# Performance work log

Measured on AMD Instinct MI355X. Metric: run time of the kernel, lower is better.

## Reference

```python
import jax, jax.numpy as jnp
import numpy as np

N_NODES = 50000
N_EDGES = 800000
IN_DIM = 128
HID_DIM = 256
OUT_DIM = 128


def _sage_conv(x, edge_index, W_l, b_l, W_r):
    """PyG SAGEConv with mean aggregation:
       out_i = W_l @ mean_{j in N(i)} x_j + b_l + W_r @ x_i
    edge_index: [2, E] with row 0 = source j, row 1 = target i."""
    src, dst = edge_index[0], edge_index[1]
    n = x.shape[0]
    # gather source features along edges, scatter-sum into targets
    msg_sum = jax.ops.segment_sum(x[src], dst, num_segments=n)  # [N, D]
    deg = jax.ops.segment_sum(jnp.ones((src.shape[0],), dtype=x.dtype), dst,
                              num_segments=n)                    # [N]
    msg_mean = msg_sum / jnp.maximum(deg, 1.0)[:, None]
    return msg_mean @ W_l.T + b_l + x @ W_r.T


def setup_inputs() -> dict:
    key = jax.random.key(0)
    ks = jax.random.split(key, 8)
    x = jax.random.normal(ks[0], (N_NODES, IN_DIM), dtype=jnp.float32)
    edge_index = jax.random.randint(ks[1], (2, N_EDGES), 0, N_NODES, dtype=jnp.int64)
    # glorot-ish scaled params
    def w(k, shape):
        fan_in = shape[-1]
        return jax.random.normal(k, shape, dtype=jnp.float32) / np.sqrt(fan_in)
    W1_l = w(ks[2], (HID_DIM, IN_DIM))
    W1_r = w(ks[3], (HID_DIM, IN_DIM))
    b1 = jnp.zeros((HID_DIM,), dtype=jnp.float32)
    W2_l = w(ks[4], (OUT_DIM, HID_DIM))
    W2_r = w(ks[5], (OUT_DIM, HID_DIM))
    b2 = jnp.zeros((OUT_DIM,), dtype=jnp.float32)
    return {"x": x, "edge_index": edge_index,
            "W1_l": W1_l, "b1": b1, "W1_r": W1_r,
            "W2_l": W2_l, "b2": b2, "W2_r": W2_r}


def reference(x, edge_index, W1_l, b1, W1_r, W2_l, b2, W2_r):
    h = _sage_conv(x, edge_index, W1_l, b1, W1_r)
    h = jax.nn.relu(h)
    # dropout(p=0.3) is identity in inference mode
    out = _sage_conv(h, edge_index, W2_l, b2, W2_r)
    return out
```

## Files before the change

kernel.cpp:

```cpp
#include <hip/hip_runtime.h>
#include <stdint.h>

#define NN 50000
#define NE 800000
#define NBK 512
#define NPB 98
#define BUCKCAP 2048

typedef __bf16 bf16x8 __attribute__((ext_vector_type(8)));
typedef float  f32x4  __attribute__((ext_vector_type(4)));

__device__ __forceinline__ unsigned short f2bf(float f) {
    unsigned int u = __float_as_uint(f);
    unsigned int r = (u + 0x7fffu + ((u >> 16) & 1u)) >> 16;
    return (unsigned short)r;
}
__device__ __forceinline__ float bf_lo(unsigned int v) { return __uint_as_float(v << 16); }
__device__ __forceinline__ float bf_hi(unsigned int v) { return __uint_as_float(v & 0xffff0000u); }

__device__ __forceinline__ void gl_lds16(const void* g, void* l) {
    __builtin_amdgcn_global_load_lds(
        (const __attribute__((address_space(1))) void*)g,
        (__attribute__((address_space(3))) void*)l, 16, 0, 0);
}

#define FILL_NB 391
#define PACK_NB 512
#define CAST_NB 6250
__global__ __launch_bounds__(256) void mega_kernel(
    const int* __restrict__ edges,
    int* __restrict__ bcur, unsigned int* __restrict__ packed,
    const float* __restrict__ x,
    const float* __restrict__ W1l, const float* __restrict__ W1r,
    const float* __restrict__ W2l, const float* __restrict__ W2r,
    unsigned short* __restrict__ x_bf,
    unsigned short* __restrict__ B1, unsigned short* __restrict__ B2) {
    __shared__ int hist[NBK];
    __shared__ int scn[NBK];
    __shared__ int gbase[NBK];
    __shared__ int lcur[NBK];
    __shared__ int ps[256];
    __shared__ unsigned int sortbuf[2048];
    __shared__ int gaddrbuf[2048];
    __shared__ int nz;
    int b = blockIdx.x;
    int t = threadIdx.x;
    if (b < FILL_NB) {
        const int E = NE;
        if (t == 0) nz = 0;
        hist[t] = 0; hist[t + 256] = 0;
        __syncthreads();
        int accv = 0;
        for (int i = t; i < 512; i += 256) accv |= edges[2 * i + 1];
        if (accv) atomicOr(&nz, 1);
        __syncthreads();
        int f = nz ? 0 : 1;

        int blockbase = b * 2048;
        int nedge = E - blockbase; if (nedge > 2048) nedge = 2048;
        unsigned int pk[8]; int bk[8];
#pragma unroll
        for (int u = 0; u < 8; ++u) {
            int lin = u * 256 + t;
            bk[u] = -1;
            if (lin < nedge) {
                int e = blockbase + lin;
                int src = edges[(size_t)e << f];
                int dst = edges[(size_t)(E + e) << f];
                int bb = dst / NPB;
                pk[u] = (unsigned int)src | ((unsigned int)(dst - bb * NPB) << 16);
                bk[u] = bb;
                atomicAdd(&hist[bb], 1);
            }
        }
        __syncthreads();
        int h0 = hist[2 * t], h1 = hist[2 * t + 1];
        int s = h0 + h1;
        ps[t] = s;
        __syncthreads();
        for (int off = 1; off < 256; off <<= 1) {
            int v = (t >= off) ? ps[t - off] : 0;
            __syncthreads();
            ps[t] += v;
            __syncthreads();
        }
        int excl = ps[t] - s;
        scn[2 * t] = excl;
        scn[2 * t + 1] = excl + h0;
        if (h0) gbase[2 * t] = atomicAdd(&bcur[2 * t], h0);
        if (h1) gbase[2 * t + 1] = atomicAdd(&bcur[2 * t + 1], h1);
        lcur[2 * t] = excl;
        lcur[2 * t + 1] = excl + h0;
        __syncthreads();
#pragma unroll
        for (int u = 0; u < 8; ++u) {
            if (bk[u] >= 0) {
                int p = atomicAdd(&lcur[bk[u]], 1);
                sortbuf[p] = pk[u];
                int off = gbase[bk[u]] + (p - scn[bk[u]]);
                gaddrbuf[p] = (off < BUCKCAP) ? (bk[u] * BUCKCAP + off) : -1;
            }
        }
        __syncthreads();
        for (int j = t; j < nedge; j += 256) {
            int a = gaddrbuf[j];
            if (a >= 0) packed[a] = sortbuf[j];
        }
    } else if (b < FILL_NB + PACK_NB) {
        int idx = (b - FILL_NB) * 256 + t;
        if (idx < 65536) {
            int o = idx >> 8, k = idx & 255;
            float v = (k < 128) ? W1l[o * 128 + k] : W1r[o * 128 + (k - 128)];
            B1[idx] = f2bf(v);
        } else {
            int j = idx - 65536;
            int o = j >> 8, k = j & 255;
            float v = (o < 128) ? W2l[o * 256 + k] : W2r[(o - 128) * 256 + k];
            B2[j] = f2bf(v);
        }
    } else {
        int i4 = (b - FILL_NB - PACK_NB) * 256 + t;
        float4 v = *(const float4*)(x + (size_t)i4 * 4);
        uint2 p;
        p.x = (unsigned int)f2bf(v.x) | ((unsigned int)f2bf(v.y) << 16);
        p.y = (unsigned int)f2bf(v.z) | ((unsigned int)f2bf(v.w) << 16);
        *(uint2*)(x_bf + (size_t)i4 * 4) = p;
    }
}

__global__ __launch_bounds__(256) void pass2_kernel(
    const unsigned int* __restrict__ packed, const int* __restrict__ bcur,
    int* __restrict__ nbr, int* __restrict__ row_start, int* __restrict__ deg) {
    __shared__ int hist[NPB];
    __shared__ int scn[NPB];
    __shared__ int lcur[NPB];
    int b = blockIdx.x;
    int t = threadIdx.x;
    int ne = bcur[b]; if (ne > BUCKCAP) ne = BUCKCAP;
    if (t < NPB) hist[t] = 0;
    __syncthreads();
    const unsigned int* pb = packed + (size_t)b * BUCKCAP;
    for (int j = t; j < ne; j += 256) atomicAdd(&hist[pb[j] >> 16], 1);
    __syncthreads();
    if (t == 0) {
        int a = 0;
        for (int i = 0; i < NPB; ++i) { scn[i] = a; a += hist[i]; }
    }
    __syncthreads();
    if (t < NPB) lcur[t] = scn[t];
    __syncthreads();
    for (int j = t; j < ne; j += 256) {
        unsigned int w = pb[j];
        int p = atomicAdd(&lcur[w >> 16], 1);
        nbr[(size_t)b * BUCKCAP + p] = (int)(w & 0xffffu);
    }
    if (t < NPB) {
        int node = b * NPB + t;
        if (node < NN) {
            row_start[node] = b * BUCKCAP + scn[t];
            deg[node] = hist[t];
        }
    }
}

__global__ __launch_bounds__(256) void agg1_kernel(
    const unsigned short* __restrict__ X, const int* __restrict__ row_start,
    const int* __restrict__ deg, const int* __restrict__ nbr,
    unsigned short* __restrict__ mean) {
    int node = blockIdx.x * 16 + (threadIdx.x >> 4);
    int l = threadIdx.x & 15;
    if (node >= NN) return;
    int dg = deg[node];
    const int* sl = nbr + row_start[node];
    float a0 = 0.f, a1 = 0.f, a2 = 0.f, a3 = 0.f, a4 = 0.f, a5 = 0.f, a6 = 0.f, a7 = 0.f;
    int i = 0;
    for (; i + 8 <= dg; i += 8) {
        uint4 v[8];
#pragma unroll
        for (int u = 0; u < 8; ++u) {
            int s = sl[i + u];
            v[u] = *(const uint4*)(X + ((size_t)s << 7) + l * 8);
        }
#pragma unroll
        for (int u = 0; u < 8; ++u) {
            a0 += bf_lo(v[u].x); a1 += bf_hi(v[u].x);
            a2 += bf_lo(v[u].y); a3 += bf_hi(v[u].y);
            a4 += bf_lo(v[u].z); a5 += bf_hi(v[u].z);
            a6 += bf_lo(v[u].w); a7 += bf_hi(v[u].w);
        }
    }
    for (; i < dg; ++i) {
        int s = sl[i];
        uint4 v = *(const uint4*)(X + ((size_t)s << 7) + l * 8);
        a0 += bf_lo(v.x); a1 += bf_hi(v.x);
        a2 += bf_lo(v.y); a3 += bf_hi(v.y);
        a4 += bf_lo(v.z); a5 += bf_hi(v.z);
        a6 += bf_lo(v.w); a7 += bf_hi(v.w);
    }
    float inv = 1.0f / (float)(dg > 1 ? dg : 1);
    uint4 p;
    p.x = (unsigned int)f2bf(a0 * inv) | ((unsigned int)f2bf(a1 * inv) << 16);
    p.y = (unsigned int)f2bf(a2 * inv) | ((unsigned int)f2bf(a3 * inv) << 16);
    p.z = (unsigned int)f2bf(a4 * inv) | ((unsigned int)f2bf(a5 * inv) << 16);
    p.w = (unsigned int)f2bf(a6 * inv) | ((unsigned int)f2bf(a7 * inv) << 16);
    *(uint4*)(mean + ((size_t)node << 7) + l * 8) = p;
}

__global__ __launch_bounds__(256) void gemm_mfma(
    const unsigned short* __restrict__ A1, const unsigned short* __restrict__ A2,
    int astr1, int astr2,
    const unsigned short* __restrict__ B,
    const float* __restrict__ biasBF, const float* __restrict__ biasF,
    unsigned short* __restrict__ outBF, float* __restrict__ outF,
    int N, int split, int reluBF) {
    __shared__ unsigned short As[64 * 64];
    __shared__ unsigned short Bs[256 * 64];
    int tid = threadIdx.x;
    int row0 = blockIdx.x * 64;
    int w = tid >> 6, lane = tid & 63;
    int q = lane >> 4, l16 = lane & 15;
    int rc = lane >> 3;
    int gsw = (lane & 7) ^ (rc & 7);

    f32x4 acc[4][4];
#pragma unroll
    for (int r = 0; r < 4; ++r)
#pragma unroll
        for (int c = 0; c < 4; ++c) acc[r][c] = (f32x4){0.f, 0.f, 0.f, 0.f};

    for (int ks = 0; ks < 4; ++ks) {
        int kbase = ks * 64;
        if (ks) __syncthreads();
        const unsigned short* Ap = (ks < 2) ? A1 : A2;
        int astr = (ks < 2) ? astr1 : astr2;
        int koff = (ks & 1) * 64;
#pragma unroll
        for (int cc = 0; cc < 2; ++cc) {
            int c = w * 2 + cc;
            int grow = row0 + c * 8 + rc;
            if (grow > N - 1) grow = N - 1;
            gl_lds16(Ap + (size_t)grow * astr + koff + gsw * 8, &As[c * 512]);
        }
#pragma unroll
        for (int cc = 0; cc < 8; ++cc) {
            int c = w * 8 + cc;
            int n = c * 8 + rc;
            gl_lds16(B + ((size_t)n << 8) + kbase + gsw * 8, &Bs[c * 512]);
        }
        __syncthreads();
#pragma unroll
        for (int k0 = 0; k0 < 64; k0 += 32) {
            int gb = (k0 >> 3) + q;
            int sl = gb ^ (l16 & 7);
            bf16x8 bfrag[4], afrag[4];
#pragma unroll
            for (int c = 0; c < 4; ++c) {
                int row = w * 64 + c * 16 + l16;
                bfrag[c] = *(const bf16x8*)&Bs[row * 64 + sl * 8];
            }
#pragma unroll
            for (int r = 0; r < 4; ++r) {
                int row = r * 16 + l16;
                afrag[r] = *(const bf16x8*)&As[row * 64 + sl * 8];
            }
#pragma unroll
            for (int r = 0; r < 4; ++r)
#pragma unroll
                for (int c = 0; c < 4; ++c)
                    acc[r][c] = __builtin_amdgcn_mfma_f32_16x16x32_bf16(afrag[r], bfrag[c], acc[r][c], 0, 0, 0);
        }
    }

#pragma unroll
    for (int c = 0; c < 4; ++c) {
        int colg = w * 64 + c * 16 + l16;
        bool isBF = (colg < split);
        float bb = 0.f;
        if (isBF) { if (biasBF) bb = biasBF[colg]; }
        else      bb = biasF[colg - split];
#pragma unroll
        for (int r = 0; r < 4; ++r) {
#pragma unroll
            for (int reg = 0; reg < 4; ++reg) {
                int rowg = row0 + r * 16 + q * 4 + reg;
                if (rowg < N) {
                    float v = acc[r][c][reg] + bb;
                    if (isBF) {
                        if (reluBF) v = fmaxf(v, 0.f);
                        outBF[(size_t)rowg * split + colg] = f2bf(v);
                    } else {
                        outF[(size_t)rowg * (256 - split) + (colg - split)] = v;
                    }
                }
            }
        }
    }
}

__global__ __launch_bounds__(256) void agg2_kernel(
    const unsigned short* __restrict__ P, const float* __restrict__ R,
    const int* __restrict__ row_start, const int* __restrict__ deg,
    const int* __restrict__ nbr, float* __restrict__ out) {
    int node = blockIdx.x * 16 + (threadIdx.x >> 4);
    int l = threadIdx.x & 15;
    if (node >= NN) return;
    int dg = deg[node];
    const int* sl = nbr + row_start[node];
    float a0 = 0.f, a1 = 0.f, a2 = 0.f, a3 = 0.f, a4 = 0.f, a5 = 0.f, a6 = 0.f, a7 = 0.f;
    int i = 0;
    for (; i + 8 <= dg; i += 8) {
        uint4 v[8];
#pragma unroll
        for (int u = 0; u < 8; ++u) {
            int s = sl[i + u];
            v[u] = *(const uint4*)(P + ((size_t)s << 7) + l * 8);
        }
#pragma unroll
        for (int u = 0; u < 8; ++u) {
            a0 += bf_lo(v[u].x); a1 += bf_hi(v[u].x);
            a2 += bf_lo(v[u].y); a3 += bf_hi(v[u].y);
            a4 += bf_lo(v[u].z); a5 += bf_hi(v[u].z);
            a6 += bf_lo(v[u].w); a7 += bf_hi(v[u].w);
        }
    }
    for (; i < dg; ++i) {
        int s = sl[i];
        uint4 v = *(const uint4*)(P + ((size_t)s << 7) + l * 8);
        a0 += bf_lo(v.x); a1 += bf_hi(v.x);
        a2 += bf_lo(v.y); a3 += bf_hi(v.y);
        a4 += bf_lo(v.z); a5 += bf_hi(v.z);
        a6 += bf_lo(v.w); a7 += bf_hi(v.w);
    }
    float inv = 1.0f / (float)(dg > 1 ? dg : 1);
    const float* rrow = R + ((size_t)node << 7) + l * 8;
    float4 r0 = *(const float4*)rrow;
    float4 r1 = *(const float4*)(rrow + 4);
    float4 o0, o1;
    o0.x = a0 * inv + r0.x; o0.y = a1 * inv + r0.y;
    o0.z = a2 * inv + r0.z; o0.w = a3 * inv + r0.w;
    o1.x = a4 * inv + r1.x; o1.y = a5 * inv + r1.y;
    o1.z = a6 * inv + r1.z; o1.w = a7 * inv + r1.w;
    float* orow = out + ((size_t)node << 7) + l * 8;
    *(float4*)orow = o0;
    *(float4*)(orow + 4) = o1;
}

extern "C" void kernel_launch(void* const* d_in, const int* in_sizes, int n_in,
                              void* d_out, int out_size, void* d_ws, size_t ws_size,
                              hipStream_t stream) {
    const float* x    = (const float*)d_in[0];
    const int*   edges = (const int*)d_in[1];
    const float* W1_l = (const float*)d_in[2];
    const float* b1   = (const float*)d_in[3];
    const float* W1_r = (const float*)d_in[4];
    const float* W2_l = (const float*)d_in[5];
    const float* b2   = (const float*)d_in[6];
    const float* W2_r = (const float*)d_in[7];
    float* out = (float*)d_out;

    const int N = NN;
    auto al = [](size_t v) { return (v + 255) & ~(size_t)255; };
    char* ws = (char*)d_ws;
    size_t o = 0;
    int* bcur = (int*)(ws + o); o += al((size_t)NBK * 4);
    unsigned int* packed = (unsigned int*)(ws + o); o += al((size_t)NBK * BUCKCAP * 4);
    int* nbr       = (int*)(ws + o); o += al((size_t)NBK * BUCKCAP * 4);
    int* row_start = (int*)(ws + o); o += al((size_t)N * 4);
    int* deg       = (int*)(ws + o); o += al((size_t)N * 4);
    unsigned short* x_bf  = (unsigned short*)(ws + o); o += al((size_t)N * 128 * 2);
    unsigned short* mean1 = (unsigned short*)(ws + o); o += al((size_t)N * 128 * 2);
    unsigned short* h_bf  = (unsigned short*)(ws + o); o += al((size_t)N * 256 * 2);
    unsigned short* P_bf  = (unsigned short*)(ws + o); o += al((size_t)N * 128 * 2);
    float*          R_f   = (float*)(ws + o);          o += al((size_t)N * 128 * 4);
    unsigned short* B1    = (unsigned short*)(ws + o); o += al((size_t)256 * 256 * 2);
    unsigned short* B2    = (unsigned short*)(ws + o); o += al((size_t)256 * 256 * 2);

    hipMemsetAsync(bcur, 0, (size_t)NBK * 4, stream);
    mega_kernel<<<FILL_NB + PACK_NB + CAST_NB, 256, 0, stream>>>(
        edges, bcur, packed, x, W1_l, W1_r, W2_l, W2_r, x_bf, B1, B2);
    pass2_kernel<<<NBK, 256, 0, stream>>>(packed, bcur, nbr, row_start, deg);
    agg1_kernel<<<(N + 15) / 16, 256, 0, stream>>>(x_bf, row_start, deg, nbr, mean1);
    gemm_mfma<<<(N + 63) / 64, 256, 0, stream>>>(mean1, x_bf, 128, 128, B1, b1, b1,
                                                 h_bf, (float*)nullptr, N, 256, 1);
    gemm_mfma<<<(N + 63) / 64, 256, 0, stream>>>(h_bf, h_bf + 128, 256, 256, B2,
                                                 (float*)nullptr, b2, P_bf, R_f, N, 128, 0);
    agg2_kernel<<<(N + 15) / 16, 256, 0, stream>>>(P_bf, R_f, row_start, deg, nbr, out);
}
```

Baseline: 251.5 us.

## Fuse CSR bucket sort with layer-1 aggregation and shrink neighbor indices to 16-bit

Merges the per-bucket counting sort with the first mean aggregation into one 512-thread kernel. The sorted neighbor lists stay in LDS and are read from there during aggregation, so that step no longer re-reads neighbor indices from global memory. Neighbor indices are now stored as 16-bit local offsets, which halves the index traffic for the second aggregation. The memset and weight packing move into a small prep kernel, removing one launch overall. The trade-off is that the fused kernel has only 512 blocks, which may cut parallelism for the gather-heavy aggregation.

```diff
diff --git a/kernel.cpp b/kernel.cpp
--- a/kernel.cpp
+++ b/kernel.cpp
@@ -24,17 +24,35 @@
         (__attribute__((address_space(3))) void*)l, 16, 0, 0);
 }
 
+__global__ __launch_bounds__(256) void prep_kernel(
+    int* __restrict__ bcur,
+    const float* __restrict__ W1l, const float* __restrict__ W1r,
+    const float* __restrict__ W2l, const float* __restrict__ W2r,
+    unsigned short* __restrict__ B1, unsigned short* __restrict__ B2) {
+    int b = blockIdx.x, t = threadIdx.x;
+    if (b == 0) {
+        bcur[t] = 0; bcur[t + 256] = 0;
+    } else {
+        int idx = (b - 1) * 256 + t;
+        if (idx < 65536) {
+            int o = idx >> 8, k = idx & 255;
+            float v = (k < 128) ? W1l[o * 128 + k] : W1r[o * 128 + (k - 128)];
+            B1[idx] = f2bf(v);
+        } else {
+            int j = idx - 65536;
+            int o = j >> 8, k = j & 255;
+            float v = (o < 128) ? W2l[o * 256 + k] : W2r[(o - 128) * 256 + k];
+            B2[j] = f2bf(v);
+        }
+    }
+}
+
 #define FILL_NB 391
-#define PACK_NB 512
 #define CAST_NB 6250
 __global__ __launch_bounds__(256) void mega_kernel(
     const int* __restrict__ edges,
     int* __restrict__ bcur, unsigned int* __restrict__ packed,
-    const float* __restrict__ x,
-    const float* __restrict__ W1l, const float* __restrict__ W1r,
-    const float* __restrict__ W2l, const float* __restrict__ W2r,
-    unsigned short* __restrict__ x_bf,
-    unsigned short* __restrict__ B1, unsigned short* __restrict__ B2) {
+    const float* __restrict__ x, unsigned short* __restrict__ x_bf) {
     __shared__ int hist[NBK];
     __shared__ int scn[NBK];
     __shared__ int gbase[NBK];
@@ -106,20 +124,8 @@
             int a = gaddrbuf[j];
             if (a >= 0) packed[a] = sortbuf[j];
         }
-    } else if (b < FILL_NB + PACK_NB) {
-        int idx = (b - FILL_NB) * 256 + t;
-        if (idx < 65536) {
-            int o = idx >> 8, k = idx & 255;
-            float v = (k < 128) ? W1l[o * 128 + k] : W1r[o * 128 + (k - 128)];
-            B1[idx] = f2bf(v);
-        } else {
-            int j = idx - 65536;
-            int o = j >> 8, k = j & 255;
-            float v = (o < 128) ? W2l[o * 256 + k] : W2r[(o - 128) * 256 + k];
-            B2[j] = f2bf(v);
-        }
     } else {
-        int i4 = (b - FILL_NB - PACK_NB) * 256 + t;
+        int i4 = (b - FILL_NB) * 256 + t;
         float4 v = *(const float4*)(x + (size_t)i4 * 4);
         uint2 p;
         p.x = (unsigned int)f2bf(v.x) | ((unsigned int)f2bf(v.y) << 16);
@@ -128,19 +134,22 @@
     }
 }
 
-__global__ __launch_bounds__(256) void pass2_kernel(
+__global__ __launch_bounds__(512) void pass2agg1_kernel(
     const unsigned int* __restrict__ packed, const int* __restrict__ bcur,
-    int* __restrict__ nbr, int* __restrict__ row_start, int* __restrict__ deg) {
+    const unsigned short* __restrict__ X,
+    unsigned short* __restrict__ nbr, int* __restrict__ row_start, int* __restrict__ deg,
+    unsigned short* __restrict__ mean) {
     __shared__ int hist[NPB];
     __shared__ int scn[NPB];
     __shared__ int lcur[NPB];
+    __shared__ unsigned short lists[BUCKCAP];
     int b = blockIdx.x;
     int t = threadIdx.x;
     int ne = bcur[b]; if (ne > BUCKCAP) ne = BUCKCAP;
     if (t < NPB) hist[t] = 0;
     __syncthreads();
     const unsigned int* pb = packed + (size_t)b * BUCKCAP;
-    for (int j = t; j < ne; j += 256) atomicAdd(&hist[pb[j] >> 16], 1);
+    for (int j = t; j < ne; j += 512) atomicAdd(&hist[pb[j] >> 16], 1);
     __syncthreads();
     if (t == 0) {
         int a = 0;
@@ -149,11 +158,12 @@
     __syncthreads();
     if (t < NPB) lcur[t] = scn[t];
     __syncthreads();
-    for (int j = t; j < ne; j += 256) {
+    for (int j = t; j < ne; j += 512) {
         unsigned int w = pb[j];
         int p = atomicAdd(&lcur[w >> 16], 1);
-        nbr[(size_t)b * BUCKCAP + p] = (int)(w & 0xffffu);
-    }
+        lists[p] = (unsigned short)(w & 0xffffu);
+    }
+    __syncthreads();
     if (t < NPB) {
         int node = b * NPB + t;
         if (node < NN) {
@@ -161,49 +171,47 @@
             deg[node] = hist[t];
         }
     }
-}
-
-__global__ __launch_bounds__(256) void agg1_kernel(
-    const unsigned short* __restrict__ X, const int* __restrict__ row_start,
-    const int* __restrict__ deg, const int* __restrict__ nbr,
-    unsigned short* __restrict__ mean) {
-    int node = blockIdx.x * 16 + (threadIdx.x >> 4);
-    int l = threadIdx.x & 15;
-    if (node >= NN) return;
-    int dg = deg[node];
-    const int* sl = nbr + row_start[node];
-    float a0 = 0.f, a1 = 0.f, a2 = 0.f, a3 = 0.f, a4 = 0.f, a5 = 0.f, a6 = 0.f, a7 = 0.f;
-    int i = 0;
-    for (; i + 8 <= dg; i += 8) {
-        uint4 v[8];
-#pragma unroll
-        for (int u = 0; u < 8; ++u) {
-            int s = sl[i + u];
-            v[u] = *(const uint4*)(X + ((size_t)s << 7) + l * 8);
-        }
-#pragma unroll
-        for (int u = 0; u < 8; ++u) {
-            a0 += bf_lo(v[u].x); a1 += bf_hi(v[u].x);
-            a2 += bf_lo(v[u].y); a3 += bf_hi(v[u].y);
-            a4 += bf_lo(v[u].z); a5 += bf_hi(v[u].z);
-            a6 += bf_lo(v[u].w); a7 += bf_hi(v[u].w);
-        }
-    }
-    for (; i < dg; ++i) {
-        int s = sl[i];
-        uint4 v = *(const uint4*)(X + ((size_t)s << 7) + l * 8);
-        a0 += bf_lo(v.x); a1 += bf_hi(v.x);
-        a2 += bf_lo(v.y); a3 += bf_hi(v.y);
-        a4 += bf_lo(v.z); a5 += bf_hi(v.z);
-        a6 += bf_lo(v.w); a7 += bf_hi(v.w);
-    }
-    float inv = 1.0f / (float)(dg > 1 ? dg : 1);
-    uint4 p;
-    p.x = (unsigned int)f2bf(a0 * inv) | ((unsigned int)f2bf(a1 * inv) << 16);
-    p.y = (unsigned int)f2bf(a2 * inv) | ((unsigned int)f2bf(a3 * inv) << 16);
-    p.z = (unsigned int)f2bf(a4 * inv) | ((unsigned int)f2bf(a5 * inv) << 16);
-    p.w = (unsigned int)f2bf(a6 * inv) | ((unsigned int)f2bf(a7 * inv) << 16);
-    *(uint4*)(mean + ((size_t)node << 7) + l * 8) = p;
+    for (int j = t; j < ne; j += 512) nbr[(size_t)b * BUCKCAP + j] = lists[j];
+    int qw = t >> 4;
+    int l = t & 15;
+    for (int n = qw; n < NPB; n += 32) {
+        int node = b * NPB + n;
+        if (node >= NN) break;
+        int dg = hist[n];
+        const unsigned short* sl = &lists[scn[n]];
+        float a0 = 0.f, a1 = 0.f, a2 = 0.f, a3 = 0.f, a4 = 0.f, a5 = 0.f, a6 = 0.f, a7 = 0.f;
+        int i = 0;
+        for (; i + 8 <= dg; i += 8) {
+            uint4 v[8];
+#pragma unroll
+            for (int u = 0; u < 8; ++u) {
+                int s = sl[i + u];
+                v[u] = *(const uint4*)(X + ((size_t)s << 7) + l * 8);
+            }
+#pragma unroll
+            for (int u = 0; u < 8; ++u) {
+                a0 += bf_lo(v[u].x); a1 += bf_hi(v[u].x);
+                a2 += bf_lo(v[u].y); a3 += bf_hi(v[u].y);
+                a4 += bf_lo(v[u].z); a5 += bf_hi(v[u].z);
+                a6 += bf_lo(v[u].w); a7 += bf_hi(v[u].w);
+            }
+        }
+        for (; i < dg; ++i) {
+            int s = sl[i];
+            uint4 v = *(const uint4*)(X + ((size_t)s << 7) + l * 8);
+            a0 += bf_lo(v.x); a1 += bf_hi(v.x);
+            a2 += bf_lo(v.y); a3 += bf_hi(v.y);
+            a4 += bf_lo(v.z); a5 += bf_hi(v.z);
+            a6 += bf_lo(v.w); a7 += bf_hi(v.w);
+        }
+        float inv = 1.0f / (float)(dg > 1 ? dg : 1);
+        uint4 p;
+        p.x = (unsigned int)f2bf(a0 * inv) | ((unsigned int)f2bf(a1 * inv) << 16);
+        p.y = (unsigned int)f2bf(a2 * inv) | ((unsigned int)f2bf(a3 * inv) << 16);
+        p.z = (unsigned int)f2bf(a4 * inv) | ((unsigned int)f2bf(a5 * inv) << 16);
+        p.w = (unsigned int)f2bf(a6 * inv) | ((unsigned int)f2bf(a7 * inv) << 16);
+        *(uint4*)(mean + ((size_t)node << 7) + l * 8) = p;
+    }
 }
 
 __global__ __launch_bounds__(256) void gemm_mfma(
@@ -300,12 +308,12 @@
 __global__ __launch_bounds__(256) void agg2_kernel(
     const unsigned short* __restrict__ P, const float* __restrict__ R,
     const int* __restrict__ row_start, const int* __restrict__ deg,
-    const int* __restrict__ nbr, float* __restrict__ out) {
+    const unsigned short* __restrict__ nbr, float* __restrict__ out) {
     int node = blockIdx.x * 16 + (threadIdx.x >> 4);
     int l = threadIdx.x & 15;
     if (node >= NN) return;
     int dg = deg[node];
-    const int* sl = nbr + row_start[node];
+    const unsigned short* sl = nbr + row_start[node];
     float a0 = 0.f, a1 = 0.f, a2 = 0.f, a3 = 0.f, a4 = 0.f, a5 = 0.f, a6 = 0.f, a7 = 0.f;
     int i = 0;
     for (; i + 8 <= dg; i += 8) {
@@ -364,7 +372,7 @@
     size_t o = 0;
     int* bcur = (int*)(ws + o); o += al((size_t)NBK * 4);
     unsigned int* packed = (unsigned int*)(ws + o); o += al((size_t)NBK * BUCKCAP * 4);
-    int* nbr       = (int*)(ws + o); o += al((size_t)NBK * BUCKCAP * 4);
+    unsigned short* nbr = (unsigned short*)(ws + o); o += al((size_t)NBK * BUCKCAP * 2);
     int* row_start = (int*)(ws + o); o += al((size_t)N * 4);
     int* deg       = (int*)(ws + o); o += al((size_t)N * 4);
     unsigned short* x_bf  = (unsigned short*)(ws + o); o += al((size_t)N * 128 * 2);
@@ -375,11 +383,9 @@
     unsigned short* B1    = (unsigned short*)(ws + o); o += al((size_t)256 * 256 * 2);
     unsigned short* B2    = (unsigned short*)(ws + o); o += al((size_t)256 * 256 * 2);
 
-    hipMemsetAsync(bcur, 0, (size_t)NBK * 4, stream);
-    mega_kernel<<<FILL_NB + PACK_NB + CAST_NB, 256, 0, stream>>>(
-        edges, bcur, packed, x, W1_l, W1_r, W2_l, W2_r, x_bf, B1, B2);
-    pass2_kernel<<<NBK, 256, 0, stream>>>(packed, bcur, nbr, row_start, deg);
-    agg1_kernel<<<(N + 15) / 16, 256, 0, stream>>>(x_bf, row_start, deg, nbr, mean1);
+    prep_kernel<<<513, 256, 0, stream>>>(bcur, W1_l, W1_r, W2_l, W2_r, B1, B2);
+    mega_kernel<<<FILL_NB + CAST_NB, 256, 0, stream>>>(edges, bcur, packed, x, x_bf);
+    pass2agg1_kernel<<<NBK, 512, 0, stream>>>(packed, bcur, x_bf, nbr, row_start, deg, mean1);
     gemm_mfma<<<(N + 63) / 64, 256, 0, stream>>>(mean1, x_bf, 128, 128, B1, b1, b1,
                                                  h_bf, (float*)nullptr, N, 256, 1);
     gemm_mfma<<<(N + 63) / 64, 256, 0, stream>>>(h_bf, h_bf + 128, 256, 256, B2,
```

After: 243.6 us. 3.1% less time.
